# Kernel tuning notes

Hardware: AMD Instinct MI355X
Metric: run time of the kernel (lower is better)

Reference implementation:

```python
import jax, jax.numpy as jnp
import numpy as np

B, S, C = 4, 2048, 1024

def setup_inputs() -> dict:
    key = jax.random.key(0)
    ks = jax.random.split(key, 9)
    lim = 1.0 / np.sqrt(C)  # torch nn.Linear default init range
    def lin_params(kw, kb):
        W = jax.random.uniform(kw, (C, C), jnp.float32, -lim, lim)
        b = jax.random.uniform(kb, (C,), jnp.float32, -lim, lim)
        return W, b
    Wq, bq = lin_params(ks[0], ks[1])
    Wk, bk = lin_params(ks[2], ks[3])
    Wv, bv = lin_params(ks[4], ks[5])
    query = jax.random.normal(ks[6], (B, S, C), jnp.float32)
    key_t = jax.random.normal(ks[7], (B, S, C), jnp.float32)
    value = jax.random.normal(ks[8], (B, S, C), jnp.float32)
    return {"query": query, "key": key_t, "value": value,
            "Wq": Wq, "bq": bq, "Wk": Wk, "bk": bk, "Wv": Wv, "bv": bv}

def reference(query, key, value, Wq, bq, Wk, bk, Wv, bv):
    # Linear projections: y = x @ W^T + b (torch Linear convention, W is [out, in])
    Q = jnp.einsum('bsc,dc->bsd', query, Wq) + bq
    K = jnp.einsum('bsc,dc->bsd', key, Wk) + bk
    V = jnp.einsum('bsc,dc->bsd', value, Wv) + bv
    scale = jnp.float32(C) ** 0.5
    scores = jnp.einsum('bqd,bkd->bqk', Q, K) / scale  # [B, S, S]
    attn = jax.nn.softmax(scores, axis=-1)
    out = jnp.einsum('bqk,bkd->bqd', attn, V)  # [B, S, C]
    return out
```

## Files before the change

kernel.cpp:

```cpp
#include <hip/hip_runtime.h>
#include <hip/hip_bf16.h>


typedef _Float16 half8 __attribute__((ext_vector_type(8)));
typedef _Float16 half4 __attribute__((ext_vector_type(4)));
typedef float f32x4 __attribute__((ext_vector_type(4)));

#define AS1(p) ((const __attribute__((address_space(1))) void*)(p))
#define AS3(p) ((__attribute__((address_space(3))) void*)(p))
#define MFMA16(a, b, c) __builtin_amdgcn_mfma_f32_16x16x32_f16(a, b, c, 0, 0, 0)

__global__ __launch_bounds__(256) void cvtw_f32_f16(
    const float* __restrict__ wq, const float* __restrict__ wk,
    const float* __restrict__ wv, _Float16* __restrict__ Wqh) {
    constexpr long WSZ = 1048576;
    const int b = blockIdx.x;
    const int tz = b >> 9;
    const float* s = tz == 0 ? wq : tz == 1 ? wk : wv;
    _Float16* d = Wqh + (long)tz * WSZ;
    const long i = (long)(b & 511) * 2048 + threadIdx.x * 8;
    float4 a = *(const float4*)(s + i);
    float4 c = *(const float4*)(s + i + 4);
    half8 h;
    h[0] = (_Float16)a.x; h[1] = (_Float16)a.y; h[2] = (_Float16)a.z; h[3] = (_Float16)a.w;
    h[4] = (_Float16)c.x; h[5] = (_Float16)c.y; h[6] = (_Float16)c.z; h[7] = (_Float16)c.w;
    *(half8*)(d + i) = h;
}

__global__ __launch_bounds__(256, 2)
void gemm_proj_a32(const float* __restrict__ X0, const float* __restrict__ X1,
                   const float* __restrict__ X2, const _Float16* __restrict__ Wh,
                   const float* __restrict__ b0, const float* __restrict__ b1,
                   const float* __restrict__ b2, _Float16* __restrict__ QKout,
                   _Float16* __restrict__ VtOut) {
    constexpr int K = 1024;
    __shared__ float AsmF[128 * 64] __attribute__((aligned(16)));
    __shared__ _Float16 Bsm[128 * 64] __attribute__((aligned(16)));
    const int tid = threadIdx.x;
    const int lane = tid & 63;
    const int wave = tid >> 6;

    const int lin = blockIdx.x;
    const int g = lin & 7;
    const int s = lin >> 3;
    const int xt = s & 7;
    const int row_id = g * 24 + (s >> 3);
    const int yt = row_id & 63;
    const int tz = row_id >> 6;
    const int m0 = yt * 128;
    const int n0 = xt * 128;

    const float* Xp = tz == 0 ? X0 : tz == 1 ? X1 : X2;
    const float* bias = tz == 0 ? b0 : tz == 1 ? b1 : b2;
    const float* Abase = Xp + (long)m0 * K;
    const _Float16* Bbase = Wh + (long)tz * 1048576 + (long)n0 * K;

    const int rin = lane >> 4;
    const int pch = lane & 15;
    const int srow8 = lane >> 3;
    const int sq = ((lane & 7) ^ srow8) << 3;
    const int quad = lane >> 4;
    const int l16 = lane & 15;
    const int wm = (wave >> 1) << 6;
    const int wn = (wave & 1) << 6;
    const int fa_base = (wm + l16) * 64;
    const int fb_base = (wn + l16) * 64;
    int chB[2];
#pragma unroll
    for (int ks = 0; ks < 2; ++ks) chB[ks] = ((ks * 4 + quad) ^ (l16 & 7)) << 3;
    int chA0[2], chA1[2];
#pragma unroll
    for (int ks = 0; ks < 2; ++ks) {
        const int f = ks * 4 + quad;
        chA0[ks] = ((2 * f) ^ l16) << 2;
        chA1[ks] = ((2 * f + 1) ^ l16) << 2;
    }

    f32x4 acc[4][4];
#pragma unroll
    for (int i = 0; i < 4; i++)
#pragma unroll
        for (int j = 0; j < 4; j++)
#pragma unroll
            for (int r = 0; r < 4; r++) acc[i][j][r] = 0.0f;

    for (int k0 = 0; k0 < K; k0 += 64) {
        __syncthreads();
#pragma unroll
        for (int u = 0; u < 8; ++u) {
            const int sl = wave + u * 4;
            const int r = sl * 4 + rin;
            const int lq = (pch ^ (r & 15)) << 2;
            __builtin_amdgcn_global_load_lds(
                AS1(Abase + (long)r * K + k0 + lq),
                AS3(AsmF + sl * 256), 16, 0, 0);
        }
#pragma unroll
        for (int u = 0; u < 4; ++u) {
            const int t = wave + u * 4;
            __builtin_amdgcn_global_load_lds(
                AS1(Bbase + (long)(t * 8 + srow8) * K + k0 + sq),
                AS3(Bsm + t * 512), 16, 0, 0);
        }
        __syncthreads();

#pragma unroll
        for (int ks = 0; ks < 2; ++ks) {
            half8 af[4], bf[4];
#pragma unroll
            for (int i = 0; i < 4; i++) {
                const f32x4 lo = *(const f32x4*)(AsmF + fa_base + i * 1024 + chA0[ks]);
                const f32x4 hi = *(const f32x4*)(AsmF + fa_base + i * 1024 + chA1[ks]);
                af[i][0] = (_Float16)lo[0]; af[i][1] = (_Float16)lo[1];
                af[i][2] = (_Float16)lo[2]; af[i][3] = (_Float16)lo[3];
                af[i][4] = (_Float16)hi[0]; af[i][5] = (_Float16)hi[1];
                af[i][6] = (_Float16)hi[2]; af[i][7] = (_Float16)hi[3];
            }
#pragma unroll
            for (int j = 0; j < 4; j++) bf[j] = *(const half8*)(Bsm + fb_base + j * 1024 + chB[ks]);
#pragma unroll
            for (int i = 0; i < 4; i++)
#pragma unroll
                for (int j = 0; j < 4; j++)
                    acc[i][j] = MFMA16(af[i], bf[j], acc[i][j]);
        }
    }

    const bool trout = (tz == 2);
#pragma unroll
    for (int i = 0; i < 4; i++) {
        const int row = m0 + wm + i * 16 + quad * 4;
#pragma unroll
        for (int j = 0; j < 4; j++) {
            const int col = n0 + wn + j * 16 + l16;
            const float badd = bias[col];
            if (trout) {
                const long b = row >> 11;
                const int sl = row & 2047;
                half4 h;
#pragma unroll
                for (int r = 0; r < 4; r++) h[r] = (_Float16)(acc[i][j][r] + badd);
                *(half4*)(VtOut + b * 2097152 + (long)col * 2048 + sl) = h;
            } else {
                _Float16* o = QKout + (long)tz * 8388608;
#pragma unroll
                for (int r = 0; r < 4; r++)
                    o[(long)(row + r) * 1024 + col] = (_Float16)(acc[i][j][r] + badd);
            }
        }
    }
}

template <int K, int NX_SH, int R, int NYT_SH, bool F16OUT>
__global__ __launch_bounds__(256, 2)
void gemm_nt(const _Float16* __restrict__ A, const _Float16* __restrict__ Bt,
             void* __restrict__ Cout, int N, float scale,
             long sA, long sB, long sC) {
    __shared__ _Float16 Asm[128 * 128] __attribute__((aligned(16)));
    __shared__ _Float16 Bsm[128 * 128] __attribute__((aligned(16)));
    const int tid = threadIdx.x;
    const int lane = tid & 63;
    const int wave = tid >> 6;

    const int lin = blockIdx.x;
    const int g = lin & 7;
    const int s = lin >> 3;
    const int xt = s & ((1 << NX_SH) - 1);
    const int row_id = g * R + (s >> NX_SH);
    const int yt = row_id & ((1 << NYT_SH) - 1);
    const int tz = row_id >> NYT_SH;
    const int m0 = yt * 128;
    const int n0 = xt * 128;

    A += (long)tz * sA;
    Bt += (long)tz * sB;

    const int rin = lane >> 4;
    const int pch = lane & 15;
    const int quad = lane >> 4;
    const int l16 = lane & 15;
    const int wm = (wave >> 1) << 6;
    const int wn = (wave & 1) << 6;
    const int fa_base = (wm + l16) * 128;
    const int fb_base = (wn + l16) * 128;
    int ch[4];
#pragma unroll
    for (int ks = 0; ks < 4; ++ks) ch[ks] = (((ks * 4 + quad) ^ l16) << 3);

    f32x4 acc[4][4];
#pragma unroll
    for (int i = 0; i < 4; i++)
#pragma unroll
        for (int j = 0; j < 4; j++)
#pragma unroll
            for (int r = 0; r < 4; r++) acc[i][j][r] = 0.0f;

    const _Float16* Abase = A + (long)m0 * K;
    const _Float16* Bbase = Bt + (long)n0 * K;

    for (int k0 = 0; k0 < K; k0 += 128) {
        __syncthreads();
#pragma unroll
        for (int u = 0; u < 16; ++u) {
            const int t = wave + u * 4;
            const int sl = t & 31;
            const int r = sl * 4 + rin;
            const int lq = (pch ^ (((sl & 3) << 2) + rin)) << 3;
            if (t < 32) {
                __builtin_amdgcn_global_load_lds(
                    AS1(Abase + (long)r * K + k0 + lq),
                    AS3(Asm + sl * 512), 16, 0, 0);
            } else {
                __builtin_amdgcn_global_load_lds(
                    AS1(Bbase + (long)r * K + k0 + lq),
                    AS3(Bsm + sl * 512), 16, 0, 0);
            }
        }
        __syncthreads();

#pragma unroll
        for (int ks = 0; ks < 4; ++ks) {
            half8 af[4], bf[4];
#pragma unroll
            for (int i = 0; i < 4; i++) af[i] = *(const half8*)(Asm + fa_base + i * 2048 + ch[ks]);
#pragma unroll
            for (int j = 0; j < 4; j++) bf[j] = *(const half8*)(Bsm + fb_base + j * 2048 + ch[ks]);
#pragma unroll
            for (int i = 0; i < 4; i++)
#pragma unroll
                for (int j = 0; j < 4; j++)
                    acc[i][j] = MFMA16(af[i], bf[j], acc[i][j]);
        }
    }

#pragma unroll
    for (int i = 0; i < 4; i++) {
        const int row = m0 + wm + i * 16 + quad * 4;
#pragma unroll
        for (int j = 0; j < 4; j++) {
            const int col = n0 + wn + j * 16 + l16;
#pragma unroll
            for (int r = 0; r < 4; r++) {
                float v = acc[i][j][r] * scale;
                if constexpr (F16OUT)
                    ((_Float16*)Cout + (long)tz * sC)[(long)(row + r) * N + col] = (_Float16)v;
                else
                    ((float*)Cout + (long)tz * sC)[(long)(row + r) * N + col] = v;
            }
        }
    }
}

__global__ __launch_bounds__(256) void softmax_f16(const _Float16* __restrict__ S,
                                                   _Float16* __restrict__ P) {
    const long row = blockIdx.x;
    const int t = threadIdx.x;
    const int wave = t >> 6, lane = t & 63;
    half8 h = ((const half8*)(S + row * 2048))[t];
    float v[8];
#pragma unroll
    for (int j = 0; j < 8; j++) v[j] = (float)h[j];
    float m = v[0];
#pragma unroll
    for (int j = 1; j < 8; j++) m = fmaxf(m, v[j]);
#pragma unroll
    for (int off = 32; off > 0; off >>= 1) m = fmaxf(m, __shfl_xor(m, off, 64));
    __shared__ float redm[4], reds[4];
    if (lane == 0) redm[wave] = m;
    __syncthreads();
    m = fmaxf(fmaxf(redm[0], redm[1]), fmaxf(redm[2], redm[3]));
    float sum = 0.0f;
#pragma unroll
    for (int j = 0; j < 8; j++) { v[j] = __expf(v[j] - m); sum += v[j]; }
#pragma unroll
    for (int off = 32; off > 0; off >>= 1) sum += __shfl_xor(sum, off, 64);
    if (lane == 0) reds[wave] = sum;
    __syncthreads();
    sum = (reds[0] + reds[1]) + (reds[2] + reds[3]);
    const float inv = 1.0f / sum;
    half8 o;
#pragma unroll
    for (int j = 0; j < 8; j++) o[j] = (_Float16)(v[j] * inv);
    ((half8*)(P + row * 2048))[t] = o;
}

extern "C" void kernel_launch(void* const* d_in, const int* in_sizes, int n_in,
                              void* d_out, int out_size, void* d_ws, size_t ws_size,
                              hipStream_t stream) {
    constexpr int B = 4, S = 2048, C = 1024;
    constexpr long XSZ = (long)B * S * C;

    const float* query = (const float*)d_in[0];
    const float* key   = (const float*)d_in[1];
    const float* value = (const float*)d_in[2];
    const float* Wq = (const float*)d_in[3];
    const float* bq = (const float*)d_in[4];
    const float* Wk = (const float*)d_in[5];
    const float* bk = (const float*)d_in[6];
    const float* Wv = (const float*)d_in[7];
    const float* bv = (const float*)d_in[8];
    float* out = (float*)d_out;
    char* ws = (char*)d_ws;

    _Float16* Wqh = (_Float16*)(ws + 50331648);
    _Float16* scores = (_Float16*)(ws + 0);
    _Float16* Qh  = (_Float16*)(ws + 73400320);
    _Float16* attn = (_Float16*)(ws + 73400320);
    _Float16* Vt  = (_Float16*)(ws + 106954752);
    if (ws_size < 123731968) return;

    cvtw_f32_f16<<<1536, 256, 0, stream>>>(Wq, Wk, Wv, Wqh);

    gemm_proj_a32<<<1536, 256, 0, stream>>>(
        query, key, value, Wqh, bq, bk, bv, Qh, Vt);

    gemm_nt<1024, 4, 8, 4, true><<<1024, 256, 0, stream>>>(
        Qh, Qh + XSZ, scores, S, 0.03125f,
        (long)S * C, (long)S * C, (long)S * S);

    softmax_f16<<<B * S, 256, 0, stream>>>(scores, attn);

    gemm_nt<2048, 3, 8, 4, false><<<512, 256, 0, stream>>>(
        attn, Vt, out, C, 1.0f,
        (long)S * S, (long)C * S, (long)S * C);
}
```

Baseline: 309.3 us.

## Pre-convert activations to fp16 and use one-wave-per-row softmax

Activations (query/key/value) are now converted to fp16 in a separate pass together with the weights, so the projection GEMM streams fp16 A tiles instead of fp32 and no longer converts inside its inner loop. This halves A-tile global and LDS traffic in the GEMM. In exchange it adds an extra read/write pass over 3x8M elements. Softmax is also restructured so each wave handles a full row with shuffles only, removing the LDS reductions and block barriers.

```diff
diff --git a/kernel.cpp b/kernel.cpp
--- a/kernel.cpp
+++ b/kernel.cpp
@@ -10,15 +10,28 @@
 #define AS3(p) ((__attribute__((address_space(3))) void*)(p))
 #define MFMA16(a, b, c) __builtin_amdgcn_mfma_f32_16x16x32_f16(a, b, c, 0, 0, 0)
 
-__global__ __launch_bounds__(256) void cvtw_f32_f16(
-    const float* __restrict__ wq, const float* __restrict__ wk,
-    const float* __restrict__ wv, _Float16* __restrict__ Wqh) {
-    constexpr long WSZ = 1048576;
+__global__ __launch_bounds__(256) void cvt6_f32_f16(
+    const float* __restrict__ q, const float* __restrict__ k,
+    const float* __restrict__ v, const float* __restrict__ wq,
+    const float* __restrict__ wk, const float* __restrict__ wv,
+    _Float16* __restrict__ Xq, _Float16* __restrict__ Wqh) {
+    constexpr long XSZ = 8388608, WSZ = 1048576;
     const int b = blockIdx.x;
-    const int tz = b >> 9;
-    const float* s = tz == 0 ? wq : tz == 1 ? wk : wv;
-    _Float16* d = Wqh + (long)tz * WSZ;
-    const long i = (long)(b & 511) * 2048 + threadIdx.x * 8;
+    const float* s;
+    _Float16* d;
+    long i;
+    if (b < 12288) {
+        const int tz = b >> 12;
+        s = tz == 0 ? q : tz == 1 ? k : v;
+        d = Xq + (long)tz * XSZ;
+        i = (long)(b & 4095) * 2048 + threadIdx.x * 8;
+    } else {
+        const int b2 = b - 12288;
+        const int tz = b2 >> 9;
+        s = tz == 0 ? wq : tz == 1 ? wk : wv;
+        d = Wqh + (long)tz * WSZ;
+        i = (long)(b2 & 511) * 2048 + threadIdx.x * 8;
+    }
     float4 a = *(const float4*)(s + i);
     float4 c = *(const float4*)(s + i + 4);
     half8 h;
@@ -28,13 +41,12 @@
 }
 
 __global__ __launch_bounds__(256, 2)
-void gemm_proj_a32(const float* __restrict__ X0, const float* __restrict__ X1,
-                   const float* __restrict__ X2, const _Float16* __restrict__ Wh,
-                   const float* __restrict__ b0, const float* __restrict__ b1,
-                   const float* __restrict__ b2, _Float16* __restrict__ QKout,
-                   _Float16* __restrict__ VtOut) {
+void gemm_proj(const _Float16* __restrict__ A, const _Float16* __restrict__ Bt,
+               const float* __restrict__ b0, const float* __restrict__ b1,
+               const float* __restrict__ b2, _Float16* __restrict__ QKout,
+               _Float16* __restrict__ VtOut) {
     constexpr int K = 1024;
-    __shared__ float AsmF[128 * 64] __attribute__((aligned(16)));
+    __shared__ _Float16 Asm[128 * 64] __attribute__((aligned(16)));
     __shared__ _Float16 Bsm[128 * 64] __attribute__((aligned(16)));
     const int tid = threadIdx.x;
     const int lane = tid & 63;
@@ -50,31 +62,20 @@
     const int m0 = yt * 128;
     const int n0 = xt * 128;
 
-    const float* Xp = tz == 0 ? X0 : tz == 1 ? X1 : X2;
     const float* bias = tz == 0 ? b0 : tz == 1 ? b1 : b2;
-    const float* Abase = Xp + (long)m0 * K;
-    const _Float16* Bbase = Wh + (long)tz * 1048576 + (long)n0 * K;
-
-    const int rin = lane >> 4;
-    const int pch = lane & 15;
+    const _Float16* Abase = A + (long)tz * 8388608 + (long)m0 * K;
+    const _Float16* Bbase = Bt + (long)tz * 1048576 + (long)n0 * K;
+
     const int srow8 = lane >> 3;
     const int sq = ((lane & 7) ^ srow8) << 3;
     const int quad = lane >> 4;
     const int l16 = lane & 15;
     const int wm = (wave >> 1) << 6;
     const int wn = (wave & 1) << 6;
-    const int fa_base = (wm + l16) * 64;
-    const int fb_base = (wn + l16) * 64;
-    int chB[2];
-#pragma unroll
-    for (int ks = 0; ks < 2; ++ks) chB[ks] = ((ks * 4 + quad) ^ (l16 & 7)) << 3;
-    int chA0[2], chA1[2];
-#pragma unroll
-    for (int ks = 0; ks < 2; ++ks) {
-        const int f = ks * 4 + quad;
-        chA0[ks] = ((2 * f) ^ l16) << 2;
-        chA1[ks] = ((2 * f + 1) ^ l16) << 2;
-    }
+    const int fa0 = (wm + l16) * 64 + (((0 * 4 + quad) ^ (l16 & 7)) << 3);
+    const int fa1 = (wm + l16) * 64 + (((1 * 4 + quad) ^ (l16 & 7)) << 3);
+    const int fb0 = (wn + l16) * 64 + (((0 * 4 + quad) ^ (l16 & 7)) << 3);
+    const int fb1 = (wn + l16) * 64 + (((1 * 4 + quad) ^ (l16 & 7)) << 3);
 
     f32x4 acc[4][4];
 #pragma unroll
@@ -88,36 +89,28 @@
         __syncthreads();
 #pragma unroll
         for (int u = 0; u < 8; ++u) {
-            const int sl = wave + u * 4;
-            const int r = sl * 4 + rin;
-            const int lq = (pch ^ (r & 15)) << 2;
-            __builtin_amdgcn_global_load_lds(
-                AS1(Abase + (long)r * K + k0 + lq),
-                AS3(AsmF + sl * 256), 16, 0, 0);
-        }
-#pragma unroll
-        for (int u = 0; u < 4; ++u) {
             const int t = wave + u * 4;
-            __builtin_amdgcn_global_load_lds(
-                AS1(Bbase + (long)(t * 8 + srow8) * K + k0 + sq),
-                AS3(Bsm + t * 512), 16, 0, 0);
+            if (t < 16) {
+                __builtin_amdgcn_global_load_lds(
+                    AS1(Abase + (long)(t * 8 + srow8) * K + k0 + sq),
+                    AS3(Asm + t * 512), 16, 0, 0);
+            } else {
+                __builtin_amdgcn_global_load_lds(
+                    AS1(Bbase + (long)((t - 16) * 8 + srow8) * K + k0 + sq),
+                    AS3(Bsm + (t - 16) * 512), 16, 0, 0);
+            }
         }
         __syncthreads();
 
 #pragma unroll
         for (int ks = 0; ks < 2; ++ks) {
+            const int ao = ks ? fa1 : fa0;
+            const int bo = ks ? fb1 : fb0;
             half8 af[4], bf[4];
 #pragma unroll
-            for (int i = 0; i < 4; i++) {
-                const f32x4 lo = *(const f32x4*)(AsmF + fa_base + i * 1024 + chA0[ks]);
-                const f32x4 hi = *(const f32x4*)(AsmF + fa_base + i * 1024 + chA1[ks]);
-                af[i][0] = (_Float16)lo[0]; af[i][1] = (_Float16)lo[1];
-                af[i][2] = (_Float16)lo[2]; af[i][3] = (_Float16)lo[3];
-                af[i][4] = (_Float16)hi[0]; af[i][5] = (_Float16)hi[1];
-                af[i][6] = (_Float16)hi[2]; af[i][7] = (_Float16)hi[3];
-            }
-#pragma unroll
-            for (int j = 0; j < 4; j++) bf[j] = *(const half8*)(Bsm + fb_base + j * 1024 + chB[ks]);
+            for (int i = 0; i < 4; i++) af[i] = *(const half8*)(Asm + ao + i * 1024);
+#pragma unroll
+            for (int j = 0; j < 4; j++) bf[j] = *(const half8*)(Bsm + bo + j * 1024);
 #pragma unroll
             for (int i = 0; i < 4; i++)
 #pragma unroll
@@ -251,37 +244,43 @@
     }
 }
 
-__global__ __launch_bounds__(256) void softmax_f16(const _Float16* __restrict__ S,
-                                                   _Float16* __restrict__ P) {
-    const long row = blockIdx.x;
-    const int t = threadIdx.x;
-    const int wave = t >> 6, lane = t & 63;
-    half8 h = ((const half8*)(S + row * 2048))[t];
-    float v[8];
-#pragma unroll
-    for (int j = 0; j < 8; j++) v[j] = (float)h[j];
+__global__ __launch_bounds__(256) void softmax4_f16(const _Float16* __restrict__ S,
+                                                    _Float16* __restrict__ P) {
+    const int wave = threadIdx.x >> 6;
+    const int lane = threadIdx.x & 63;
+    const long row = (long)blockIdx.x * 4 + wave;
+    const _Float16* src = S + row * 2048;
+    _Float16* dst = P + row * 2048;
+
+    half8 h[4];
+#pragma unroll
+    for (int u = 0; u < 4; u++) h[u] = ((const half8*)src)[lane + 64 * u];
+    float v[32];
+#pragma unroll
+    for (int u = 0; u < 4; u++)
+#pragma unroll
+        for (int j = 0; j < 8; j++) v[u * 8 + j] = (float)h[u][j];
+
     float m = v[0];
 #pragma unroll
-    for (int j = 1; j < 8; j++) m = fmaxf(m, v[j]);
+    for (int e = 1; e < 32; e++) m = fmaxf(m, v[e]);
 #pragma unroll
     for (int off = 32; off > 0; off >>= 1) m = fmaxf(m, __shfl_xor(m, off, 64));
-    __shared__ float redm[4], reds[4];
-    if (lane == 0) redm[wave] = m;
-    __syncthreads();
-    m = fmaxf(fmaxf(redm[0], redm[1]), fmaxf(redm[2], redm[3]));
+
     float sum = 0.0f;
 #pragma unroll
-    for (int j = 0; j < 8; j++) { v[j] = __expf(v[j] - m); sum += v[j]; }
+    for (int e = 0; e < 32; e++) { v[e] = __expf(v[e] - m); sum += v[e]; }
 #pragma unroll
     for (int off = 32; off > 0; off >>= 1) sum += __shfl_xor(sum, off, 64);
-    if (lane == 0) reds[wave] = sum;
-    __syncthreads();
-    sum = (reds[0] + reds[1]) + (reds[2] + reds[3]);
     const float inv = 1.0f / sum;
-    half8 o;
-#pragma unroll
-    for (int j = 0; j < 8; j++) o[j] = (_Float16)(v[j] * inv);
-    ((half8*)(P + row * 2048))[t] = o;
+
+#pragma unroll
+    for (int u = 0; u < 4; u++) {
+        half8 o;
+#pragma unroll
+        for (int j = 0; j < 8; j++) o[j] = (_Float16)(v[u * 8 + j] * inv);
+        ((half8*)dst)[lane + 64 * u] = o;
+    }
 }
 
 extern "C" void kernel_launch(void* const* d_in, const int* in_sizes, int n_in,
@@ -302,23 +301,25 @@
     float* out = (float*)d_out;
     char* ws = (char*)d_ws;
 
-    _Float16* Wqh = (_Float16*)(ws + 50331648);
+    _Float16* Xq  = (_Float16*)(ws + 0);
+    _Float16* Wqh = (_Float16*)(ws + 3 * XSZ * 2);
     _Float16* scores = (_Float16*)(ws + 0);
     _Float16* Qh  = (_Float16*)(ws + 73400320);
     _Float16* attn = (_Float16*)(ws + 73400320);
     _Float16* Vt  = (_Float16*)(ws + 106954752);
     if (ws_size < 123731968) return;
 
-    cvtw_f32_f16<<<1536, 256, 0, stream>>>(Wq, Wk, Wv, Wqh);
-
-    gemm_proj_a32<<<1536, 256, 0, stream>>>(
-        query, key, value, Wqh, bq, bk, bv, Qh, Vt);
+    cvt6_f32_f16<<<13824, 256, 0, stream>>>(
+        query, key, value, Wq, Wk, Wv, Xq, Wqh);
+
+    gemm_proj<<<1536, 256, 0, stream>>>(
+        Xq, Wqh, bq, bk, bv, Qh, Vt);
 
     gemm_nt<1024, 4, 8, 4, true><<<1024, 256, 0, stream>>>(
         Qh, Qh + XSZ, scores, S, 0.03125f,
         (long)S * C, (long)S * C, (long)S * S);
 
-    softmax_f16<<<B * S, 256, 0, stream>>>(scores, attn);
+    softmax4_f16<<<B * S / 4, 256, 0, stream>>>(scores, attn);
 
     gemm_nt<2048, 3, 8, 4, false><<<512, 256, 0, stream>>>(
         attn, Vt, out, C, 1.0f,
```

Result: faster. 299.5 us, median of 2 (-3.2%).
